# Optimization experiments

Measured on AMD Instinct MI355X. Metric: run time of the kernel, lower is better.

Reference implementation:

```python
import jax, jax.numpy as jnp
import numpy as np

B = 8192
N_COLS = 64
D = 1024
EPS = 1e-5


def _layernorm(x, g, b):
    m = jnp.mean(x, axis=-1, keepdims=True)
    v = jnp.mean(jnp.square(x - m), axis=-1, keepdims=True)
    return (x - m) * jax.lax.rsqrt(v + EPS) * g + b


def setup_inputs() -> dict:
    key = jax.random.key(0)
    ks = jax.random.split(key, 8)
    s = 0.02
    return {
        "x1_enc": jax.random.normal(ks[0], (1, N_COLS, D), jnp.float32),
        "x2_enc": jax.random.normal(ks[1], (B, D), jnp.float32),
        "We": jax.random.normal(ks[2], (4, 2 * D, D), jnp.float32) * s,
        "be": jnp.zeros((4, D), jnp.float32),
        "W1": jax.random.normal(ks[3], (2 * D, 4 * D), jnp.float32) * s,
        "b1": jnp.zeros((4 * D,), jnp.float32),
        "g1": jnp.ones((4 * D,), jnp.float32),
        "bt1": jnp.zeros((4 * D,), jnp.float32),
        "W2": jax.random.normal(ks[4], (4 * D, 2 * D), jnp.float32) * s,
        "b2": jnp.zeros((2 * D,), jnp.float32),
        "g2": jnp.ones((2 * D,), jnp.float32),
        "bt2": jnp.zeros((2 * D,), jnp.float32),
        "W3": jax.random.normal(ks[5], (2 * D, 1), jnp.float32) * s,
        "b3": jnp.zeros((1,), jnp.float32),
        "col_pairs": jax.random.randint(ks[6], (B, 2), 0, N_COLS, jnp.int64),
        "vis_type": jax.random.randint(ks[7], (B,), 0, 4, jnp.int64),
    }


def reference(x1_enc, x2_enc, We, be, W1, b1, g1, bt1, W2, b2, g2, bt2, W3, b3,
              col_pairs, vis_type):
    # x1 repeated B times is identical per row -> gather directly from x1_enc[0]
    x11 = x1_enc[0, col_pairs[:, 0]]          # [B, D]
    x12 = x1_enc[0, col_pairs[:, 1]]          # [B, D]
    x1c = jnp.concatenate([x11, x12], axis=1)  # [B, 2D]

    # 1-of-4 expert routing: compute all experts, select by vis_type
    all_y = jax.nn.relu(jnp.einsum('bd,edk->bek', x1c, We) + be)  # [B, 4, D]
    y1 = jnp.take_along_axis(all_y, vis_type[:, None, None], axis=1)[:, 0]  # [B, D]

    y = jnp.concatenate([y1, x2_enc], axis=1)  # [B, 2D]
    h = _layernorm(jax.nn.relu(y @ W1 + b1), g1, bt1)
    h = _layernorm(jax.nn.relu(h @ W2 + b2), g2, bt2)
    return jax.nn.sigmoid(h @ W3 + b3)  # [B, 1]
```

## Files before the change

### kernel.cpp

```cpp
#include <hip/hip_runtime.h>

typedef unsigned short u16;
typedef __bf16 bf16x8 __attribute__((ext_vector_type(8)));
typedef float f32x4v __attribute__((ext_vector_type(4)));
typedef u16 u16x8 __attribute__((ext_vector_type(8)));

__device__ __forceinline__ u16 f2bf(float f) {
  union { float f; unsigned u; } v; v.f = f;
  unsigned r = v.u + 0x7fffu + ((v.u >> 16) & 1u);
  return (u16)(r >> 16);
}
__device__ __forceinline__ float bf2f(u16 h) {
  union { unsigned u; float f; } v; v.u = ((unsigned)h) << 16;
  return v.f;
}

#define G2L16(g, l)                                                            \
  __builtin_amdgcn_global_load_lds((__attribute__((address_space(1))) void*)(g), \
                                   (__attribute__((address_space(3))) void*)(l), 16, 0, 0)

__global__ __launch_bounds__(256) void k_transpose2(const float* __restrict__ W1,
                                                    u16* __restrict__ W1T,
                                                    const float* __restrict__ W2,
                                                    u16* __restrict__ W2gT,
                                                    const float* __restrict__ g1,
                                                    const float* __restrict__ bt1,
                                                    float* __restrict__ w2ps,
                                                    float* __restrict__ w2pc) {
  __shared__ float tile[64][65];
  int bid = blockIdx.x;
  const float* in;
  u16* out;
  int R, C, bx, by, fold;
  if (bid < 2048) {
    in = W1; out = W1T; R = 2048; C = 4096; fold = 0;
    bx = bid & 63; by = bid >> 6;
  } else {
    bid -= 2048;
    in = W2; out = W2gT; R = 4096; C = 2048; fold = 1;
    bx = bid & 31; by = bid >> 5;
  }
  const int c0 = bx * 64, r0 = by * 64;
  const int t = threadIdx.x;
  const int tc = (t & 15) * 4, tr = t >> 4;
#pragma unroll
  for (int i = 0; i < 4; ++i) {
    int r = tr + i * 16;
    f32x4v v = *(const f32x4v*)(in + (size_t)(r0 + r) * C + c0 + tc);
    tile[r][tc] = v[0]; tile[r][tc + 1] = v[1];
    tile[r][tc + 2] = v[2]; tile[r][tc + 3] = v[3];
  }
  __syncthreads();
  const int oc = t >> 2;
  const int rb = (t & 3) * 16;
  float gv[16];
#pragma unroll
  for (int i = 0; i < 16; ++i) gv[i] = fold ? g1[r0 + rb + i] : 1.f;
  u16x8 o0, o1;
#pragma unroll
  for (int i = 0; i < 8; ++i) o0[i] = f2bf(tile[rb + i][oc] * gv[i]);
#pragma unroll
  for (int i = 0; i < 8; ++i) o1[i] = f2bf(tile[rb + 8 + i][oc] * gv[8 + i]);
  *(u16x8*)(out + (size_t)(c0 + oc) * R + r0 + rb) = o0;
  *(u16x8*)(out + (size_t)(c0 + oc) * R + r0 + rb + 8) = o1;
  if (fold) {
    float ps = 0.f, pc = 0.f;
#pragma unroll
    for (int i = 0; i < 16; ++i) {
      float w = tile[rb + i][oc];
      ps += gv[i] * w;
      pc += bt1[r0 + rb + i] * w;
    }
    ps += __shfl_down(ps, 2, 4); ps += __shfl_down(ps, 1, 4);
    pc += __shfl_down(pc, 2, 4); pc += __shfl_down(pc, 1, 4);
    if ((t & 3) == 0) {
      w2ps[(size_t)by * 2048 + c0 + oc] = ps;
      w2pc[(size_t)by * 2048 + c0 + oc] = pc;
    }
  }
}

__global__ __launch_bounds__(256) void k_pq(const float* __restrict__ x1,
                                            const float* __restrict__ We,
                                            float* __restrict__ pq0,
                                            float* __restrict__ pq1) {
  const int n0 = blockIdx.x * 64;
  const int ep = blockIdx.y;
  const int e = ep >> 1, p = ep & 1;
  const int ks = blockIdx.z * 512;
  float* pq = blockIdx.z ? pq1 : pq0;
  __shared__ float As[64][33];
  __shared__ float Bs[32][68];
  const int t = threadIdx.x;
  const int tx = t & 15, ty = t >> 4;
  float acc[4][4] = {};
  const float* wbase = We + (size_t)e * 2048 * 1024 + (size_t)p * 1024 * 1024;
  for (int k0 = ks; k0 < ks + 512; k0 += 32) {
#pragma unroll
    for (int i = 0; i < 8; ++i) {
      int idx = t + i * 256;
      As[idx >> 5][idx & 31] = x1[(size_t)(idx >> 5) * 1024 + k0 + (idx & 31)];
    }
#pragma unroll
    for (int i = 0; i < 8; ++i) {
      int idx = t + i * 256;
      Bs[idx >> 6][idx & 63] = wbase[(size_t)(k0 + (idx >> 6)) * 1024 + n0 + (idx & 63)];
    }
    __syncthreads();
#pragma unroll
    for (int kk = 0; kk < 32; ++kk) {
      float av[4];
#pragma unroll
      for (int i = 0; i < 4; ++i) av[i] = As[ty * 4 + i][kk];
      f32x4v bv = *(const f32x4v*)&Bs[kk][tx * 4];
#pragma unroll
      for (int i = 0; i < 4; ++i)
#pragma unroll
        for (int j = 0; j < 4; ++j) acc[i][j] += av[i] * bv[j];
    }
    __syncthreads();
  }
#pragma unroll
  for (int i = 0; i < 4; ++i) {
    float* dst = pq + ((size_t)ep * 64 + ty * 4 + i) * 1024 + n0 + tx * 4;
#pragma unroll
    for (int j = 0; j < 4; ++j) dst[j] = acc[i][j];
  }
}

__global__ __launch_bounds__(256) void k_build_y(const float* __restrict__ pq0,
                                                 const float* __restrict__ pq1,
                                                 const float* __restrict__ x2,
                                                 const float* __restrict__ be,
                                                 const int* __restrict__ cp,
                                                 const int* __restrict__ vis,
                                                 u16* __restrict__ Y) {
  const int t = threadIdx.x;
  for (int rr = 0; rr < 8; ++rr) {
    const int b = blockIdx.x * 8 + rr;
    const int e = vis[b];
    u16x8 o;
    if (t < 128) {
      const int c0 = cp[2 * b], c1 = cp[2 * b + 1];
      const size_t po = ((size_t)(e * 2) * 64 + c0) * 1024 + t * 8;
      const size_t qo = ((size_t)(e * 2 + 1) * 64 + c1) * 1024 + t * 8;
      const float* B = be + e * 1024 + t * 8;
#pragma unroll
      for (int i = 0; i < 8; ++i) {
        float v = pq0[po + i] + pq1[po + i] + pq0[qo + i] + pq1[qo + i] + B[i];
        o[i] = f2bf(v > 0.f ? v : 0.f);
      }
      *(u16x8*)(Y + (size_t)b * 2048 + t * 8) = o;
    } else {
      const float* X = x2 + (size_t)b * 1024 + (size_t)(t - 128) * 8;
#pragma unroll
      for (int i = 0; i < 8; ++i) o[i] = f2bf(X[i]);
      *(u16x8*)(Y + (size_t)b * 2048 + 1024 + (size_t)(t - 128) * 8) = o;
    }
  }
}

#define LOADAB(ASP, BSP)                                                       \
  {                                                                            \
    G2L16(aA, (ASP));                                                          \
    G2L16(aA + (size_t)32 * K, (ASP) + 2048);                                  \
    G2L16(aA + (size_t)64 * K, (ASP) + 4096);                                  \
    G2L16(aA + (size_t)96 * K, (ASP) + 6144);                                  \
    G2L16(bB, (BSP));                                                          \
    G2L16(bB + (size_t)32 * K, (BSP) + 2048);                                  \
    G2L16(bB + (size_t)64 * K, (BSP) + 4096);                                  \
    G2L16(bB + (size_t)96 * K, (BSP) + 6144);                                  \
    aA += 64; bB += 64;                                                        \
  }

#define COMPUTE(ASB, BSB)                                                      \
  {                                                                            \
    bf16x8 af[4], bfr[4];                                                      \
    _Pragma("unroll") for (int mi = 0; mi < 4; ++mi)                           \
        af[mi] = *(const bf16x8*)((ASB) + (am + mi * 16) * 64 + kp0);          \
    _Pragma("unroll") for (int ni = 0; ni < 4; ++ni)                           \
        bfr[ni] = *(const bf16x8*)((BSB) + (bn + ni * 16) * 64 + kp0);         \
    _Pragma("unroll") for (int mi = 0; mi < 4; ++mi)                           \
        _Pragma("unroll") for (int ni = 0; ni < 4; ++ni)                       \
            acc[mi][ni] = __builtin_amdgcn_mfma_f32_16x16x32_bf16(             \
                af[mi], bfr[ni], acc[mi][ni], 0, 0, 0);                        \
    _Pragma("unroll") for (int mi = 0; mi < 4; ++mi)                           \
        af[mi] = *(const bf16x8*)((ASB) + (am + mi * 16) * 64 + kp1);          \
    _Pragma("unroll") for (int ni = 0; ni < 4; ++ni)                           \
        bfr[ni] = *(const bf16x8*)((BSB) + (bn + ni * 16) * 64 + kp1);         \
    _Pragma("unroll") for (int mi = 0; mi < 4; ++mi)                           \
        _Pragma("unroll") for (int ni = 0; ni < 4; ++ni)                       \
            acc[mi][ni] = __builtin_amdgcn_mfma_f32_16x16x32_bf16(             \
                af[mi], bfr[ni], acc[mi][ni], 0, 0, 0);                        \
  }

template <int MODE>
__global__ __launch_bounds__(256) void k_gemm(const u16* __restrict__ A,
                                              const u16* __restrict__ BT,
                                              const float* __restrict__ bias,
                                              const float2* __restrict__ stats,
                                              const float* __restrict__ s1,
                                              const float* __restrict__ c1b,
                                              float2* __restrict__ sp_out,
                                              u16* __restrict__ C, int M, int N, int K) {
  __shared__ u16 As0[128 * 64];
  __shared__ u16 As1[128 * 64];
  __shared__ u16 Bs0[128 * 64];
  __shared__ u16 Bs1[128 * 64];
  const int tid = threadIdx.x;
  const int lane = tid & 63;
  const int wave = tid >> 6;

  const int nx = gridDim.x, ny = gridDim.y;
  const int bid = blockIdx.y * nx + blockIdx.x;
  const int stripe = ny >> 3;
  const int xcd = bid & 7;
  const int loc = bid >> 3;
  const int panel = loc / (stripe * 4);
  const int rem = loc - panel * (stripe * 4);
  const int by = xcd * stripe + (rem >> 2);
  const int bx = panel * 4 + (rem & 3);
  const int tileN = bx * 128;
  const int tileM = by * 128;
  const int wm = wave & 1;
  const int wn = wave >> 1;

  f32x4v acc[4][4];
#pragma unroll
  for (int i = 0; i < 4; ++i)
#pragma unroll
    for (int j = 0; j < 4; ++j) acc[i][j] = (f32x4v){0.f, 0.f, 0.f, 0.f};

  const int srow = tid >> 3;
  const int lchunk = (tid & 7) ^ (srow & 7);
  const u16* aA = A + (size_t)(tileM + srow) * K + lchunk * 8;
  const u16* bB = BT + (size_t)(tileN + srow) * K + lchunk * 8;
  u16* asp0 = As0 + tid * 8;
  u16* asp1 = As1 + tid * 8;
  u16* bsp0 = Bs0 + tid * 8;
  u16* bsp1 = Bs1 + tid * 8;

  const int s = lane & 7;
  const int kp0 = ((lane >> 4) ^ s) * 8;
  const int kp1 = kp0 ^ 32;
  const int am = wm * 64 + (lane & 15);
  const int bn = wn * 64 + (lane & 15);

  const int n = K >> 6;
  LOADAB(asp0, bsp0);
  __syncthreads();
  for (int it = 0; it < n; it += 2) {
    LOADAB(asp1, bsp1);
    COMPUTE(As0, Bs0);
    __syncthreads();
    if (it + 2 < n) LOADAB(asp0, bsp0);
    COMPUTE(As1, Bs1);
    __syncthreads();
  }

  const int crow = tileM + wm * 64 + (lane >> 4) * 4;
  const int ccol = tileN + wn * 64 + (lane & 15);
  float cv0[4], cv1[4];
#pragma unroll
  for (int ni = 0; ni < 4; ++ni) {
    const int c = ccol + ni * 16;
    if (MODE == 0) {
      cv0[ni] = bias[c];
    } else {
      cv0[ni] = s1[c];
      cv1[ni] = c1b[c];
    }
  }
  const int cb = bx * 2 + wn;
#pragma unroll
  for (int mi = 0; mi < 4; ++mi) {
#pragma unroll
    for (int r = 0; r < 4; ++r) {
      const int row = crow + mi * 16 + r;
      float m = 0.f, rs = 0.f;
      if (MODE == 1) {
        float2 st = stats[row];
        m = st.x; rs = st.y;
      }
      float s_ = 0.f, ss_ = 0.f;
#pragma unroll
      for (int ni = 0; ni < 4; ++ni) {
        float v;
        if (MODE == 0)
          v = acc[mi][ni][r] + cv0[ni];
        else
          v = rs * acc[mi][ni][r] - rs * m * cv0[ni] + cv1[ni];
        v = v > 0.f ? v : 0.f;
        if (MODE == 0) { s_ += v; ss_ += v * v; }
        C[(size_t)row * N + ccol + ni * 16] = f2bf(v);
      }
      if (MODE == 0) {
#pragma unroll
        for (int off = 8; off >= 1; off >>= 1) {
          s_ += __shfl_xor(s_, off, 16);
          ss_ += __shfl_xor(ss_, off, 16);
        }
        if ((lane & 15) == 0)
          sp_out[(size_t)cb * 8192 + row] = make_float2(s_, ss_);
      }
    }
  }
}

__global__ __launch_bounds__(256) void k_reduce(const float2* __restrict__ sp,
                                                float2* __restrict__ stats,
                                                const float* __restrict__ w2ps,
                                                const float* __restrict__ w2pc,
                                                const float* __restrict__ b2,
                                                float* __restrict__ s1,
                                                float* __restrict__ c1b) {
  const int bid = blockIdx.x;
  if (bid < 32) {
    const int row = bid * 256 + threadIdx.x;
    float s = 0.f, ss = 0.f;
    for (int cbk = 0; cbk < 64; ++cbk) {
      float2 p = sp[(size_t)cbk * 8192 + row];
      s += p.x; ss += p.y;
    }
    float m = s * (1.f / 4096.f);
    float var = ss * (1.f / 4096.f) - m * m;
    stats[row] = make_float2(m, rsqrtf(var + 1e-5f));
  } else {
    const int nn = (bid - 32) * 256 + threadIdx.x;
    float s = 0.f, c = 0.f;
    for (int kb = 0; kb < 64; ++kb) {
      s += w2ps[(size_t)kb * 2048 + nn];
      c += w2pc[(size_t)kb * 2048 + nn];
    }
    s1[nn] = s;
    c1b[nn] = c + b2[nn];
  }
}

__global__ __launch_bounds__(256) void k_ln_final(const u16* __restrict__ H2,
                                                  const float* __restrict__ g,
                                                  const float* __restrict__ bt,
                                                  const float* __restrict__ W3,
                                                  const float* __restrict__ b3,
                                                  float* __restrict__ out) {
  const int lane = threadIdx.x & 63;
  const int b = blockIdx.x * 4 + (threadIdx.x >> 6);
  const u16* row = H2 + (size_t)b * 2048;
  float vals[4][8];
  float s = 0.f, ss = 0.f;
#pragma unroll
  for (int c = 0; c < 4; ++c) {
    u16x8 v = *(const u16x8*)(row + c * 512 + lane * 8);
#pragma unroll
    for (int i = 0; i < 8; ++i) {
      float f = bf2f(v[i]);
      vals[c][i] = f;
      s += f;
      ss += f * f;
    }
  }
#pragma unroll
  for (int off = 32; off > 0; off >>= 1) {
    s += __shfl_down(s, off, 64);
    ss += __shfl_down(ss, off, 64);
  }
  s = __shfl(s, 0);
  ss = __shfl(ss, 0);
  const float m = s * (1.f / 2048.f);
  const float rs = rsqrtf(ss * (1.f / 2048.f) - m * m + 1e-5f);
  float dot = 0.f;
#pragma unroll
  for (int c = 0; c < 4; ++c)
#pragma unroll
    for (int i = 0; i < 8; ++i) {
      int col = c * 512 + lane * 8 + i;
      float h = (vals[c][i] - m) * rs * g[col] + bt[col];
      dot += h * W3[col];
    }
#pragma unroll
  for (int off = 32; off > 0; off >>= 1) dot += __shfl_down(dot, off, 64);
  if (lane == 0) out[b] = 1.f / (1.f + expf(-(dot + b3[0])));
}

extern "C" void kernel_launch(void* const* d_in, const int* in_sizes, int n_in,
                              void* d_out, int out_size, void* d_ws, size_t ws_size,
                              hipStream_t stream) {
  const float* x1 = (const float*)d_in[0];
  const float* x2 = (const float*)d_in[1];
  const float* We = (const float*)d_in[2];
  const float* be = (const float*)d_in[3];
  const float* W1 = (const float*)d_in[4];
  const float* b1 = (const float*)d_in[5];
  const float* g1 = (const float*)d_in[6];
  const float* bt1 = (const float*)d_in[7];
  const float* W2 = (const float*)d_in[8];
  const float* b2 = (const float*)d_in[9];
  const float* g2 = (const float*)d_in[10];
  const float* bt2 = (const float*)d_in[11];
  const float* W3 = (const float*)d_in[12];
  const float* b3 = (const float*)d_in[13];
  const int* cp = (const int*)d_in[14];
  const int* vis = (const int*)d_in[15];
  float* out = (float*)d_out;

  char* ws = (char*)d_ws;
  u16* W1T  = (u16*)(ws);
  u16* W2gT = (u16*)(ws + 16777216);
  u16* Y    = (u16*)(ws + 33554432);
  u16* H1   = (u16*)(ws + 67108864);
  float* PQ0 = (float*)(ws + 134217728);
  float* PQ1 = (float*)(ws + 136314880);
  float2* sp = (float2*)(ws + 134217728);
  float2* stats = (float2*)(ws + 138412032);
  float* s1   = (float*)(ws + 138477568);
  float* c1b  = (float*)(ws + 138485760);
  float* w2ps = (float*)(ws + 138493952);
  float* w2pc = (float*)(ws + 139018240);
  u16* H2 = Y;

  k_transpose2<<<4096, 256, 0, stream>>>(W1, W1T, W2, W2gT, g1, bt1, w2ps, w2pc);
  k_pq<<<dim3(16, 8, 2), 256, 0, stream>>>(x1, We, PQ0, PQ1);
  k_build_y<<<1024, 256, 0, stream>>>(PQ0, PQ1, x2, be, cp, vis, Y);
  k_gemm<0><<<dim3(32, 64), 256, 0, stream>>>(
      Y, W1T, b1, nullptr, nullptr, nullptr, sp, H1, 8192, 4096, 2048);
  k_reduce<<<40, 256, 0, stream>>>(sp, stats, w2ps, w2pc, b2, s1, c1b);
  k_gemm<1><<<dim3(16, 64), 256, 0, stream>>>(
      H1, W2gT, nullptr, stats, s1, c1b, nullptr, H2, 8192, 2048, 4096);
  k_ln_final<<<2048, 256, 0, stream>>>(H2, g2, bt2, W3, b3, out);
}
```

Measured before the change: 508.3 us.

## Merge preprocessing kernels and single-buffer GEMM LDS for higher occupancy

Merges the weight transpose kernel and the expert pq GEMM into one launch that selects its work by block index, so a kernel launch goes away and the two jobs can overlap. Changes the main bf16 MFMA GEMM from double-buffered LDS with prefetch to a single buffer (32KB) with launch_bounds(256,3), so more blocks fit per CU. The trade is that global-to-LDS loads no longer overlap the MFMA work inside a block, leaving latency hiding to the other resident blocks.

```diff
diff --git a/kernel.cpp b/kernel.cpp
--- a/kernel.cpp
+++ b/kernel.cpp
@@ -19,112 +19,115 @@
   __builtin_amdgcn_global_load_lds((__attribute__((address_space(1))) void*)(g), \
                                    (__attribute__((address_space(3))) void*)(l), 16, 0, 0)
 
-__global__ __launch_bounds__(256) void k_transpose2(const float* __restrict__ W1,
-                                                    u16* __restrict__ W1T,
-                                                    const float* __restrict__ W2,
-                                                    u16* __restrict__ W2gT,
-                                                    const float* __restrict__ g1,
-                                                    const float* __restrict__ bt1,
-                                                    float* __restrict__ w2ps,
-                                                    float* __restrict__ w2pc) {
-  __shared__ float tile[64][65];
+__global__ __launch_bounds__(256) void k_pre(const float* __restrict__ W1,
+                                             u16* __restrict__ W1T,
+                                             const float* __restrict__ W2,
+                                             u16* __restrict__ W2gT,
+                                             const float* __restrict__ g1,
+                                             const float* __restrict__ bt1,
+                                             float* __restrict__ w2ps,
+                                             float* __restrict__ w2pc,
+                                             const float* __restrict__ x1,
+                                             const float* __restrict__ We,
+                                             float* __restrict__ pq0,
+                                             float* __restrict__ pq1) {
+  __shared__ char smem[17536];
+  const int t = threadIdx.x;
   int bid = blockIdx.x;
-  const float* in;
-  u16* out;
-  int R, C, bx, by, fold;
-  if (bid < 2048) {
-    in = W1; out = W1T; R = 2048; C = 4096; fold = 0;
-    bx = bid & 63; by = bid >> 6;
+  if (bid < 4096) {
+    float(*tile)[65] = (float(*)[65])smem;
+    const float* in;
+    u16* out;
+    int R, C, bx, by, fold;
+    if (bid < 2048) {
+      in = W1; out = W1T; R = 2048; C = 4096; fold = 0;
+      bx = bid & 63; by = bid >> 6;
+    } else {
+      bid -= 2048;
+      in = W2; out = W2gT; R = 4096; C = 2048; fold = 1;
+      bx = bid & 31; by = bid >> 5;
+    }
+    const int c0 = bx * 64, r0 = by * 64;
+    const int tc = (t & 15) * 4, tr = t >> 4;
+#pragma unroll
+    for (int i = 0; i < 4; ++i) {
+      int r = tr + i * 16;
+      f32x4v v = *(const f32x4v*)(in + (size_t)(r0 + r) * C + c0 + tc);
+      tile[r][tc] = v[0]; tile[r][tc + 1] = v[1];
+      tile[r][tc + 2] = v[2]; tile[r][tc + 3] = v[3];
+    }
+    __syncthreads();
+    const int oc = t >> 2;
+    const int rb = (t & 3) * 16;
+    float gv[16];
+#pragma unroll
+    for (int i = 0; i < 16; ++i) gv[i] = fold ? g1[r0 + rb + i] : 1.f;
+    u16x8 o0, o1;
+#pragma unroll
+    for (int i = 0; i < 8; ++i) o0[i] = f2bf(tile[rb + i][oc] * gv[i]);
+#pragma unroll
+    for (int i = 0; i < 8; ++i) o1[i] = f2bf(tile[rb + 8 + i][oc] * gv[8 + i]);
+    *(u16x8*)(out + (size_t)(c0 + oc) * R + r0 + rb) = o0;
+    *(u16x8*)(out + (size_t)(c0 + oc) * R + r0 + rb + 8) = o1;
+    if (fold) {
+      float ps = 0.f, pc = 0.f;
+#pragma unroll
+      for (int i = 0; i < 16; ++i) {
+        float w = tile[rb + i][oc];
+        ps += gv[i] * w;
+        pc += bt1[r0 + rb + i] * w;
+      }
+      ps += __shfl_down(ps, 2, 4); ps += __shfl_down(ps, 1, 4);
+      pc += __shfl_down(pc, 2, 4); pc += __shfl_down(pc, 1, 4);
+      if ((t & 3) == 0) {
+        w2ps[(size_t)by * 2048 + c0 + oc] = ps;
+        w2pc[(size_t)by * 2048 + c0 + oc] = pc;
+      }
+    }
   } else {
-    bid -= 2048;
-    in = W2; out = W2gT; R = 4096; C = 2048; fold = 1;
-    bx = bid & 31; by = bid >> 5;
-  }
-  const int c0 = bx * 64, r0 = by * 64;
-  const int t = threadIdx.x;
-  const int tc = (t & 15) * 4, tr = t >> 4;
-#pragma unroll
-  for (int i = 0; i < 4; ++i) {
-    int r = tr + i * 16;
-    f32x4v v = *(const f32x4v*)(in + (size_t)(r0 + r) * C + c0 + tc);
-    tile[r][tc] = v[0]; tile[r][tc + 1] = v[1];
-    tile[r][tc + 2] = v[2]; tile[r][tc + 3] = v[3];
-  }
-  __syncthreads();
-  const int oc = t >> 2;
-  const int rb = (t & 3) * 16;
-  float gv[16];
-#pragma unroll
-  for (int i = 0; i < 16; ++i) gv[i] = fold ? g1[r0 + rb + i] : 1.f;
-  u16x8 o0, o1;
-#pragma unroll
-  for (int i = 0; i < 8; ++i) o0[i] = f2bf(tile[rb + i][oc] * gv[i]);
-#pragma unroll
-  for (int i = 0; i < 8; ++i) o1[i] = f2bf(tile[rb + 8 + i][oc] * gv[8 + i]);
-  *(u16x8*)(out + (size_t)(c0 + oc) * R + r0 + rb) = o0;
-  *(u16x8*)(out + (size_t)(c0 + oc) * R + r0 + rb + 8) = o1;
-  if (fold) {
-    float ps = 0.f, pc = 0.f;
-#pragma unroll
-    for (int i = 0; i < 16; ++i) {
-      float w = tile[rb + i][oc];
-      ps += gv[i] * w;
-      pc += bt1[r0 + rb + i] * w;
-    }
-    ps += __shfl_down(ps, 2, 4); ps += __shfl_down(ps, 1, 4);
-    pc += __shfl_down(pc, 2, 4); pc += __shfl_down(pc, 1, 4);
-    if ((t & 3) == 0) {
-      w2ps[(size_t)by * 2048 + c0 + oc] = ps;
-      w2pc[(size_t)by * 2048 + c0 + oc] = pc;
-    }
-  }
-}
-
-__global__ __launch_bounds__(256) void k_pq(const float* __restrict__ x1,
-                                            const float* __restrict__ We,
-                                            float* __restrict__ pq0,
-                                            float* __restrict__ pq1) {
-  const int n0 = blockIdx.x * 64;
-  const int ep = blockIdx.y;
-  const int e = ep >> 1, p = ep & 1;
-  const int ks = blockIdx.z * 512;
-  float* pq = blockIdx.z ? pq1 : pq0;
-  __shared__ float As[64][33];
-  __shared__ float Bs[32][68];
-  const int t = threadIdx.x;
-  const int tx = t & 15, ty = t >> 4;
-  float acc[4][4] = {};
-  const float* wbase = We + (size_t)e * 2048 * 1024 + (size_t)p * 1024 * 1024;
-  for (int k0 = ks; k0 < ks + 512; k0 += 32) {
-#pragma unroll
-    for (int i = 0; i < 8; ++i) {
-      int idx = t + i * 256;
-      As[idx >> 5][idx & 31] = x1[(size_t)(idx >> 5) * 1024 + k0 + (idx & 31)];
-    }
-#pragma unroll
-    for (int i = 0; i < 8; ++i) {
-      int idx = t + i * 256;
-      Bs[idx >> 6][idx & 63] = wbase[(size_t)(k0 + (idx >> 6)) * 1024 + n0 + (idx & 63)];
-    }
-    __syncthreads();
-#pragma unroll
-    for (int kk = 0; kk < 32; ++kk) {
-      float av[4];
-#pragma unroll
-      for (int i = 0; i < 4; ++i) av[i] = As[ty * 4 + i][kk];
-      f32x4v bv = *(const f32x4v*)&Bs[kk][tx * 4];
-#pragma unroll
-      for (int i = 0; i < 4; ++i)
-#pragma unroll
-        for (int j = 0; j < 4; ++j) acc[i][j] += av[i] * bv[j];
-    }
-    __syncthreads();
-  }
-#pragma unroll
-  for (int i = 0; i < 4; ++i) {
-    float* dst = pq + ((size_t)ep * 64 + ty * 4 + i) * 1024 + n0 + tx * 4;
-#pragma unroll
-    for (int j = 0; j < 4; ++j) dst[j] = acc[i][j];
+    const int idx = bid - 4096;
+    const int n0 = (idx & 15) * 64;
+    const int ep = (idx >> 4) & 7;
+    const int e = ep >> 1, p = ep & 1;
+    const int z = idx >> 7;
+    const int ks = z * 512;
+    float* pq = z ? pq1 : pq0;
+    float(*As)[33] = (float(*)[33])smem;
+    float(*Bs)[68] = (float(*)[68])(smem + 8448);
+    const int tx = t & 15, ty = t >> 4;
+    float acc[4][4] = {};
+    const float* wbase = We + (size_t)e * 2048 * 1024 + (size_t)p * 1024 * 1024;
+    for (int k0 = ks; k0 < ks + 512; k0 += 32) {
+#pragma unroll
+      for (int i = 0; i < 8; ++i) {
+        int ix = t + i * 256;
+        As[ix >> 5][ix & 31] = x1[(size_t)(ix >> 5) * 1024 + k0 + (ix & 31)];
+      }
+#pragma unroll
+      for (int i = 0; i < 8; ++i) {
+        int ix = t + i * 256;
+        Bs[ix >> 6][ix & 63] = wbase[(size_t)(k0 + (ix >> 6)) * 1024 + n0 + (ix & 63)];
+      }
+      __syncthreads();
+#pragma unroll
+      for (int kk = 0; kk < 32; ++kk) {
+        float av[4];
+#pragma unroll
+        for (int i = 0; i < 4; ++i) av[i] = As[ty * 4 + i][kk];
+        f32x4v bv = *(const f32x4v*)&Bs[kk][tx * 4];
+#pragma unroll
+        for (int i = 0; i < 4; ++i)
+#pragma unroll
+          for (int j = 0; j < 4; ++j) acc[i][j] += av[i] * bv[j];
+      }
+      __syncthreads();
+    }
+#pragma unroll
+    for (int i = 0; i < 4; ++i) {
+      float* dst = pq + ((size_t)ep * 64 + ty * 4 + i) * 1024 + n0 + tx * 4;
+#pragma unroll
+      for (int j = 0; j < 4; ++j) dst[j] = acc[i][j];
+    }
   }
 }
 
@@ -160,53 +163,17 @@
   }
 }
 
-#define LOADAB(ASP, BSP)                                                       \
-  {                                                                            \
-    G2L16(aA, (ASP));                                                          \
-    G2L16(aA + (size_t)32 * K, (ASP) + 2048);                                  \
-    G2L16(aA + (size_t)64 * K, (ASP) + 4096);                                  \
-    G2L16(aA + (size_t)96 * K, (ASP) + 6144);                                  \
-    G2L16(bB, (BSP));                                                          \
-    G2L16(bB + (size_t)32 * K, (BSP) + 2048);                                  \
-    G2L16(bB + (size_t)64 * K, (BSP) + 4096);                                  \
-    G2L16(bB + (size_t)96 * K, (BSP) + 6144);                                  \
-    aA += 64; bB += 64;                                                        \
-  }
-
-#define COMPUTE(ASB, BSB)                                                      \
-  {                                                                            \
-    bf16x8 af[4], bfr[4];                                                      \
-    _Pragma("unroll") for (int mi = 0; mi < 4; ++mi)                           \
-        af[mi] = *(const bf16x8*)((ASB) + (am + mi * 16) * 64 + kp0);          \
-    _Pragma("unroll") for (int ni = 0; ni < 4; ++ni)                           \
-        bfr[ni] = *(const bf16x8*)((BSB) + (bn + ni * 16) * 64 + kp0);         \
-    _Pragma("unroll") for (int mi = 0; mi < 4; ++mi)                           \
-        _Pragma("unroll") for (int ni = 0; ni < 4; ++ni)                       \
-            acc[mi][ni] = __builtin_amdgcn_mfma_f32_16x16x32_bf16(             \
-                af[mi], bfr[ni], acc[mi][ni], 0, 0, 0);                        \
-    _Pragma("unroll") for (int mi = 0; mi < 4; ++mi)                           \
-        af[mi] = *(const bf16x8*)((ASB) + (am + mi * 16) * 64 + kp1);          \
-    _Pragma("unroll") for (int ni = 0; ni < 4; ++ni)                           \
-        bfr[ni] = *(const bf16x8*)((BSB) + (bn + ni * 16) * 64 + kp1);         \
-    _Pragma("unroll") for (int mi = 0; mi < 4; ++mi)                           \
-        _Pragma("unroll") for (int ni = 0; ni < 4; ++ni)                       \
-            acc[mi][ni] = __builtin_amdgcn_mfma_f32_16x16x32_bf16(             \
-                af[mi], bfr[ni], acc[mi][ni], 0, 0, 0);                        \
-  }
-
 template <int MODE>
-__global__ __launch_bounds__(256) void k_gemm(const u16* __restrict__ A,
-                                              const u16* __restrict__ BT,
-                                              const float* __restrict__ bias,
-                                              const float2* __restrict__ stats,
-                                              const float* __restrict__ s1,
-                                              const float* __restrict__ c1b,
-                                              float2* __restrict__ sp_out,
-                                              u16* __restrict__ C, int M, int N, int K) {
-  __shared__ u16 As0[128 * 64];
-  __shared__ u16 As1[128 * 64];
-  __shared__ u16 Bs0[128 * 64];
-  __shared__ u16 Bs1[128 * 64];
+__global__ __launch_bounds__(256, 3) void k_gemm(const u16* __restrict__ A,
+                                                 const u16* __restrict__ BT,
+                                                 const float* __restrict__ bias,
+                                                 const float2* __restrict__ stats,
+                                                 const float* __restrict__ s1,
+                                                 const float* __restrict__ c1b,
+                                                 float2* __restrict__ sp_out,
+                                                 u16* __restrict__ C, int M, int N, int K) {
+  __shared__ u16 As[128 * 64];
+  __shared__ u16 Bs[128 * 64];
   const int tid = threadIdx.x;
   const int lane = tid & 63;
   const int wave = tid >> 6;
@@ -233,12 +200,10 @@
 
   const int srow = tid >> 3;
   const int lchunk = (tid & 7) ^ (srow & 7);
-  const u16* aA = A + (size_t)(tileM + srow) * K + lchunk * 8;
-  const u16* bB = BT + (size_t)(tileN + srow) * K + lchunk * 8;
-  u16* asp0 = As0 + tid * 8;
-  u16* asp1 = As1 + tid * 8;
-  u16* bsp0 = Bs0 + tid * 8;
-  u16* bsp1 = Bs1 + tid * 8;
+  const u16* aptr = A + (size_t)(tileM + srow) * K + lchunk * 8;
+  const u16* bptr = BT + (size_t)(tileN + srow) * K + lchunk * 8;
+  u16* asp = As + tid * 8;
+  u16* bsp = Bs + tid * 8;
 
   const int s = lane & 7;
   const int kp0 = ((lane >> 4) ^ s) * 8;
@@ -246,15 +211,42 @@
   const int am = wm * 64 + (lane & 15);
   const int bn = wn * 64 + (lane & 15);
 
-  const int n = K >> 6;
-  LOADAB(asp0, bsp0);
-  __syncthreads();
-  for (int it = 0; it < n; it += 2) {
-    LOADAB(asp1, bsp1);
-    COMPUTE(As0, Bs0);
+  for (int k0 = 0; k0 < K; k0 += 64) {
+    G2L16(aptr, asp);
+    G2L16(aptr + (size_t)32 * K, asp + 2048);
+    G2L16(aptr + (size_t)64 * K, asp + 4096);
+    G2L16(aptr + (size_t)96 * K, asp + 6144);
+    G2L16(bptr, bsp);
+    G2L16(bptr + (size_t)32 * K, bsp + 2048);
+    G2L16(bptr + (size_t)64 * K, bsp + 4096);
+    G2L16(bptr + (size_t)96 * K, bsp + 6144);
+    aptr += 64;
+    bptr += 64;
     __syncthreads();
-    if (it + 2 < n) LOADAB(asp0, bsp0);
-    COMPUTE(As1, Bs1);
+
+    bf16x8 af[4], bfr[4];
+#pragma unroll
+    for (int mi = 0; mi < 4; ++mi)
+      af[mi] = *(const bf16x8*)(As + (am + mi * 16) * 64 + kp0);
+#pragma unroll
+    for (int ni = 0; ni < 4; ++ni)
+      bfr[ni] = *(const bf16x8*)(Bs + (bn + ni * 16) * 64 + kp0);
+#pragma unroll
+    for (int mi = 0; mi < 4; ++mi)
+#pragma unroll
+      for (int ni = 0; ni < 4; ++ni)
+        acc[mi][ni] = __builtin_amdgcn_mfma_f32_16x16x32_bf16(af[mi], bfr[ni], acc[mi][ni], 0, 0, 0);
+#pragma unroll
+    for (int mi = 0; mi < 4; ++mi)
+      af[mi] = *(const bf16x8*)(As + (am + mi * 16) * 64 + kp1);
+#pragma unroll
+    for (int ni = 0; ni < 4; ++ni)
+      bfr[ni] = *(const bf16x8*)(Bs + (bn + ni * 16) * 64 + kp1);
+#pragma unroll
+    for (int mi = 0; mi < 4; ++mi)
+#pragma unroll
+      for (int ni = 0; ni < 4; ++ni)
+        acc[mi][ni] = __builtin_amdgcn_mfma_f32_16x16x32_bf16(af[mi], bfr[ni], acc[mi][ni], 0, 0, 0);
     __syncthreads();
   }
 
@@ -418,8 +410,8 @@
   float* w2pc = (float*)(ws + 139018240);
   u16* H2 = Y;
 
-  k_transpose2<<<4096, 256, 0, stream>>>(W1, W1T, W2, W2gT, g1, bt1, w2ps, w2pc);
-  k_pq<<<dim3(16, 8, 2), 256, 0, stream>>>(x1, We, PQ0, PQ1);
+  k_pre<<<4352, 256, 0, stream>>>(W1, W1T, W2, W2gT, g1, bt1, w2ps, w2pc,
+                                  x1, We, PQ0, PQ1);
   k_build_y<<<1024, 256, 0, stream>>>(PQ0, PQ1, x2, be, cp, vis, Y);
   k_gemm<0><<<dim3(32, 64), 256, 0, stream>>>(
       Y, W1T, b1, nullptr, nullptr, nullptr, sp, H1, 8192, 4096, 2048);
```

After: 497.6 us. 1.02x faster.
